# Performance work log

Measured on AMD Instinct MI355X. Metric: run time of the kernel, lower is better.

## Reference

```python
import jax, jax.numpy as jnp
import numpy as np

LAYERS = 30
LAYERS_PER_STACK = 10  # layers // stacks
UPSAMPLE_SCALES = (10, 8)


def _c1x1(w, x):
    # 1x1 conv: w [O,C], x [B,C,T] -> [B,O,T]
    return jnp.einsum('oc,bct->bot', w, x)


def setup_inputs() -> dict:
    key = jax.random.key(0)
    ks = jax.random.split(key, 16)
    B, T, F = 4, 32000, 400
    s = 0.1  # weight scale to keep gates unsaturated
    inp = {
        'x': jax.random.normal(ks[0], (B, 256, T), jnp.float32),
        'c': jax.random.normal(ks[1], (B, 80, F), jnp.float32),
        'first_w': jax.random.normal(ks[2], (64, 256), jnp.float32) * s,
        'first_b': jnp.zeros((64,), jnp.float32),
        'conv_w': jax.random.normal(ks[3], (LAYERS, 128, 64, 2), jnp.float32) * s,
        'conv_b': jnp.zeros((LAYERS, 128), jnp.float32),
        'cond_w': jax.random.normal(ks[4], (LAYERS, 128, 80), jnp.float32) * s,
        'out_w': jax.random.normal(ks[5], (LAYERS, 64, 64), jnp.float32) * s,
        'out_b': jnp.zeros((LAYERS, 64), jnp.float32),
        'skip_w': jax.random.normal(ks[6], (LAYERS, 64, 64), jnp.float32) * s,
        'skip_b': jnp.zeros((LAYERS, 64), jnp.float32),
        'last1_w': jax.random.normal(ks[7], (64, 64), jnp.float32) * s,
        'last1_b': jnp.zeros((64,), jnp.float32),
        'last2_w': jax.random.normal(ks[8], (256, 64), jnp.float32) * s,
        'last2_b': jnp.zeros((256,), jnp.float32),
        'conv_in_w': jax.random.normal(ks[9], (80, 80), jnp.float32) * s,
        # upsample smoothing kernels, torch init: constant 1/kernel_size
        'up_w0': jnp.full((2 * 10 + 1,), 1.0 / (2 * 10 + 1), jnp.float32),
        'up_w1': jnp.full((2 * 8 + 1,), 1.0 / (2 * 8 + 1), jnp.float32),
    }
    return inp


def _wavenet(x, c, first_w, first_b, conv_w, conv_b, cond_w, out_w, out_b,
             skip_w, skip_b, last1_w, last1_b, last2_w, last2_b, conv_in_w,
             up_w0, up_w1):
    # --- ConvInUpsampleNetwork (aux_context_window=0 -> conv_in is 1x1, no bias) ---
    c = _c1x1(conv_in_w, c)  # [B,80,F]
    C = c.shape[1]
    for scale, w in zip(UPSAMPLE_SCALES, (up_w0, up_w1)):
        c = jnp.repeat(c, scale, axis=2)  # nearest interpolate along time
        rhs = jnp.broadcast_to(w[None, None, :], (C, 1, w.shape[0]))  # depthwise avg
        c = jax.lax.conv_general_dilated(
            c, rhs, window_strides=(1,), padding=[(scale, scale)],
            feature_group_count=C, dimension_numbers=('NCH', 'OIH', 'NCH'))
    # c now [B,80,T] with T = F*80 matching x
    T = x.shape[2]

    # --- first 1x1 conv ---
    h = _c1x1(first_w, x) + first_b[None, :, None]  # [B,64,T]

    skips = jnp.zeros_like(h[:, :64, :]) * 0.0  # [B,64,T]
    skips = 0.0
    for l in range(LAYERS):
        d = 2 ** (l % LAYERS_PER_STACK)  # dilation; padding = (k-1)*d = d
        xp = jnp.pad(h, ((0, 0), (0, 0), (d, 0)))  # causal left pad
        # dilated conv, kernel_size=2: taps at t-d and t
        g = (jnp.einsum('oc,bct->bot', conv_w[l, :, :, 0], xp[:, :, :T])
             + jnp.einsum('oc,bct->bot', conv_w[l, :, :, 1], xp[:, :, d:d + T])
             + conv_b[l][None, :, None])  # [B,128,T]
        g = g + _c1x1(cond_w[l], c)  # conditioning (split(a,b)+split(ca,cb) == split(g+cc))
        a, b = jnp.split(g, 2, axis=1)
        z = jnp.tanh(a) * jax.nn.sigmoid(b)  # [B,64,T]
        skips = skips + _c1x1(skip_w[l], z) + skip_b[l][None, :, None]
        h = h + _c1x1(out_w[l], z) + out_b[l][None, :, None]

    # --- last conv layers: ReLU, 1x1, ReLU, 1x1 ---
    o = jax.nn.relu(skips)
    o = _c1x1(last1_w, o) + last1_b[None, :, None]
    o = jax.nn.relu(o)
    o = _c1x1(last2_w, o) + last2_b[None, :, None]
    return o  # [B,256,T]


def reference(x, c, first_w, first_b, conv_w, conv_b, cond_w, out_w, out_b,
              skip_w, skip_b, last1_w, last1_b, last2_w, last2_b, conv_in_w,
              up_w0, up_w1):
    return _wavenet(x, c, first_w, first_b, conv_w, conv_b, cond_w, out_w,
                    out_b, skip_w, skip_b, last1_w, last1_b, last2_w, last2_b,
                    conv_in_w, up_w0, up_w1)
```

## Files before the change

### kernel.cpp

```cpp
#include <hip/hip_runtime.h>
#include <math.h>

#define T_TOTAL 32000
#define BATCH 4
#define TT 64
#define TTF 32
#define ZCHUNK 15
#define ZSLOT_ELEMS ((size_t)BATCH * T_TOTAL * 64)

typedef __bf16 bf16x8 __attribute__((ext_vector_type(8)));
typedef float f32x4 __attribute__((ext_vector_type(4)));
typedef unsigned int uint4v __attribute__((ext_vector_type(4)));
typedef unsigned int uint2v __attribute__((ext_vector_type(2)));

__device__ __forceinline__ unsigned short f2b(float f) {
    unsigned int u = __float_as_uint(f);
    u += 0x7FFFu + ((u >> 16) & 1u);
    return (unsigned short)(u >> 16);
}
__device__ __forceinline__ unsigned int f2b2(float lo, float hi) {
    return (unsigned int)f2b(lo) | ((unsigned int)f2b(hi) << 16);
}
__device__ __forceinline__ bf16x8 ld_bf8(const unsigned short* p) {
    return __builtin_bit_cast(bf16x8, *(const uint4v*)p);
}
__device__ __forceinline__ float fast_sigmoid(float x) {
    return __builtin_amdgcn_rcpf(1.0f + __expf(-x));
}
__device__ __forceinline__ float fast_tanh(float x) {
    return 1.0f - 2.0f * __builtin_amdgcn_rcpf(1.0f + __expf(2.0f * x));
}

__global__ void k_pack(const float* __restrict__ conv_w, const float* __restrict__ cond_w,
                       const float* __restrict__ skip_w, const float* __restrict__ out_w,
                       const float* __restrict__ first_w, const float* __restrict__ last1_w,
                       const float* __restrict__ last2_w, const float* __restrict__ skip_b,
                       unsigned short* __restrict__ wgp, unsigned short* __restrict__ wzp,
                       unsigned short* __restrict__ fwp, unsigned short* __restrict__ l1p,
                       unsigned short* __restrict__ l2p, float* __restrict__ sbs) {
    int i = blockIdx.x * blockDim.x + threadIdx.x;
    if (i < 860160) {
        int l = i / 28672, r = i % 28672;
        int o = r / 224, k = r % 224;
        float v;
        if (k < 64)       v = conv_w[(((size_t)l * 128 + o) * 64 + k) * 2 + 0];
        else if (k < 128) v = conv_w[(((size_t)l * 128 + o) * 64 + (k - 64)) * 2 + 1];
        else if (k < 208) v = cond_w[((size_t)l * 128 + o) * 80 + (k - 128)];
        else              v = 0.0f;
        wgp[i] = f2b(v);
        return;
    }
    i -= 860160;
    if (i < 245760) {
        int l = i / 8192, rr = (i % 8192) / 64, k = i % 64;
        float v = (rr < 64) ? skip_w[((size_t)l * 64 + rr) * 64 + k]
                            : out_w[((size_t)l * 64 + (rr - 64)) * 64 + k];
        wzp[i] = f2b(v);
        return;
    }
    i -= 245760;
    if (i < 16384) { fwp[i] = f2b(first_w[i]); return; }
    i -= 16384;
    if (i < 4096) { l1p[i] = f2b(last1_w[i]); return; }
    i -= 4096;
    if (i < 16384) { l2p[i] = f2b(last2_w[i]); return; }
    i -= 16384;
    if (i < 64) {
        float a = 0.f;
        for (int l = 0; l < 30; ++l) a += skip_b[l * 64 + i];
        sbs[i] = a;
    }
}

__global__ void k_convin(const float* __restrict__ c, const float* __restrict__ w,
                         float* __restrict__ c1) {
    int idx = blockIdx.x * blockDim.x + threadIdx.x;
    if (idx >= BATCH * 80 * 400) return;
    int f = idx % 400;
    int o = (idx / 400) % 80;
    int b = idx / (400 * 80);
    const float* cb = c + (size_t)b * 80 * 400 + f;
    const float* wr = w + o * 80;
    float acc = 0.f;
    #pragma unroll 8
    for (int j = 0; j < 80; ++j) acc += wr[j] * cb[(size_t)j * 400];
    c1[idx] = acc;
}

__global__ void k_up0(const float* __restrict__ c1, const float* __restrict__ w,
                      float* __restrict__ c2) {
    int idx = blockIdx.x * blockDim.x + threadIdx.x;
    if (idx >= BATCH * 80 * 4000) return;
    int t = idx % 4000;
    int ch = idx / 4000;
    int u = t / 10, r = t - u * 10;
    float w0 = 0.f, w1 = 0.f, w2 = 0.f;
    #pragma unroll
    for (int j = 0; j < 21; ++j) {
        float wj = w[j];
        int a = r - 10 + j;
        if (a < 0) w0 += wj;
        else if (a < 10) w1 += wj;
        else w2 += wj;
    }
    const float* src = c1 + (size_t)ch * 400;
    float s0 = (u >= 1) ? src[u - 1] : 0.f;
    float s1 = src[u];
    float s2 = (u + 1 < 400) ? src[u + 1] : 0.f;
    c2[idx] = w0 * s0 + w1 * s1 + w2 * s2;
}

__global__ __launch_bounds__(256) void k_up1b(const float* __restrict__ c2,
                                              const float* __restrict__ w,
                                              unsigned short* __restrict__ cupb) {
    __shared__ float S[80][13];
    __shared__ float W[8][4];
    const int b = blockIdx.y, t0 = blockIdx.x * 64;
    const int tid = threadIdx.x;
    const int u0 = t0 >> 3;

    for (int i = tid; i < 800; i += 256) {
        int ch = i / 10, uu = i % 10;
        int u = u0 - 1 + uu;
        float v = 0.f;
        if (u >= 0 && u < 4000) v = c2[((size_t)b * 80 + ch) * 4000 + u];
        S[ch][uu] = v;
    }
    if (tid < 24) {
        int r = tid / 3, k = tid % 3;
        int jlo = (k == 0) ? 0 : (k == 1 ? 8 - r : 16 - r);
        int jhi = (k == 0) ? 7 - r : (k == 1 ? 15 - r : 16);
        float a = 0.f;
        for (int j = jlo; j <= jhi; ++j) a += w[j];
        W[r][k] = a;
    }
    __syncthreads();

    unsigned short* ob = cupb + ((size_t)b * T_TOTAL + t0) * 96;
    for (int i = tid; i < 64 * 96; i += 256) {
        int ch = i % 96;
        int tl = i / 96;
        float acc = 0.f;
        if (ch < 80) {
            int r = tl & 7, ub = tl >> 3;
            acc = W[r][0] * S[ch][ub] + W[r][1] * S[ch][ub + 1] + W[r][2] * S[ch][ub + 2];
        }
        ob[i] = f2b(acc);
    }
}

#define XFS 266
__global__ __launch_bounds__(256, 8) void k_first(
    const float* __restrict__ x, const unsigned short* __restrict__ fwp,
    const float* __restrict__ fb, float* __restrict__ h0) {
    __shared__ unsigned short Xf[TTF * XFS];
    const int b = blockIdx.y, t0 = blockIdx.x * TTF, tid = threadIdx.x;
    const int lane = tid & 63;
    const int wv = __builtin_amdgcn_readfirstlane(tid >> 6);
    const int l15 = lane & 15, q = lane >> 4;

    for (int i = tid; i < 2048; i += 256) {
        int ch = i >> 3;
        int t4 = (i & 7) << 2;
        const float* xr = x + ((size_t)b * 256 + ch) * T_TOTAL + t0 + t4;
        float4 u = *(const float4*)xr;
        int base = t4 * XFS + ch;
        Xf[base + 0 * XFS] = f2b(u.x);
        Xf[base + 1 * XFS] = f2b(u.y);
        Xf[base + 2 * XFS] = f2b(u.z);
        Xf[base + 3 * XFS] = f2b(u.w);
    }
    __syncthreads();

    f32x4 acc[2] = {};
    const unsigned short* wr = fwp + (size_t)(16 * wv + l15) * 256;
    #pragma unroll
    for (int ks = 0; ks < 8; ++ks) {
        bf16x8 aA = ld_bf8(wr + ks * 32 + q * 8);
        #pragma unroll
        for (int tt = 0; tt < 2; ++tt) {
            bf16x8 bb = ld_bf8(&Xf[(tt * 16 + l15) * XFS + ks * 32 + q * 8]);
            acc[tt] = __builtin_amdgcn_mfma_f32_16x16x32_bf16(aA, bb, acc[tt], 0, 0, 0);
        }
    }
    const float4 fbv = *(const float4*)&fb[16 * wv + 4 * q];
    float* hob = h0 + (size_t)b * T_TOTAL * 64;
    #pragma unroll
    for (int tt = 0; tt < 2; ++tt) {
        size_t base = (size_t)(t0 + tt * 16 + l15) * 64 + 16 * wv + 4 * q;
        float4 ho;
        ho.x = acc[tt][0] + fbv.x;
        ho.y = acc[tt][1] + fbv.y;
        ho.z = acc[tt][2] + fbv.z;
        ho.w = acc[tt][3] + fbv.w;
        *(float4*)(hob + base) = ho;
    }
}

__global__ __launch_bounds__(256, 4) void k_layer(
    const float* __restrict__ h_in, float* __restrict__ h_out,
    unsigned short* __restrict__ zb_l, const unsigned short* __restrict__ cupb,
    const unsigned short* __restrict__ wgp_l, const unsigned short* __restrict__ wzp_l,
    const float* __restrict__ cb_l, const float* __restrict__ ob_l, int d) {
    __shared__ unsigned short Xl[64 * 224];
    __shared__ unsigned short zs[64 * 72];
    const int b = blockIdx.y, t0 = blockIdx.x * TT, tid = threadIdx.x;
    const int lane = tid & 63;
    const int wv = __builtin_amdgcn_readfirstlane(tid >> 6);
    const int l15 = lane & 15, q = lane >> 4;

    const float* hb = h_in + (size_t)b * T_TOTAL * 64;
    for (int i = tid; i < 512; i += 256) {
        int t = i >> 3, cb8 = (i & 7) << 3;
        const float4* p1 = (const float4*)(hb + (size_t)(t0 + t) * 64 + cb8);
        float4 u0 = p1[0], u1 = p1[1];
        uint4v v1;
        v1.x = f2b2(u0.x, u0.y); v1.y = f2b2(u0.z, u0.w);
        v1.z = f2b2(u1.x, u1.y); v1.w = f2b2(u1.z, u1.w);
        *(uint4v*)&Xl[t * 224 + 64 + cb8] = v1;
        int td = t0 + t - d;
        uint4v v0 = {0u, 0u, 0u, 0u};
        if (td >= 0) {
            const float4* p0 = (const float4*)(hb + (size_t)td * 64 + cb8);
            float4 w0 = p0[0], w1 = p0[1];
            v0.x = f2b2(w0.x, w0.y); v0.y = f2b2(w0.z, w0.w);
            v0.z = f2b2(w1.x, w1.y); v0.w = f2b2(w1.z, w1.w);
        }
        *(uint4v*)&Xl[t * 224 + cb8] = v0;
    }
    const unsigned short* cbb = cupb + (size_t)b * T_TOTAL * 96;
    for (int i = tid; i < 768; i += 256) {
        int t = i / 12, j = (i % 12) << 3;
        *(uint4v*)&Xl[t * 224 + 128 + j] = *(const uint4v*)&cbb[(size_t)(t0 + t) * 96 + j];
    }
    __syncthreads();

    f32x4 accA[4] = {}, accG[4] = {};
    const unsigned short* wrow_a = wgp_l + (size_t)(16 * wv + l15) * 224;
    const unsigned short* wrow_g = wgp_l + (size_t)(64 + 16 * wv + l15) * 224;
    #pragma unroll
    for (int ks = 0; ks < 7; ++ks) {
        bf16x8 aA = ld_bf8(wrow_a + ks * 32 + q * 8);
        bf16x8 aG = ld_bf8(wrow_g + ks * 32 + q * 8);
        #pragma unroll
        for (int tt = 0; tt < 4; ++tt) {
            bf16x8 bb = ld_bf8(&Xl[(tt * 16 + l15) * 224 + ks * 32 + q * 8]);
            accA[tt] = __builtin_amdgcn_mfma_f32_16x16x32_bf16(aA, bb, accA[tt], 0, 0, 0);
            accG[tt] = __builtin_amdgcn_mfma_f32_16x16x32_bf16(aG, bb, accG[tt], 0, 0, 0);
        }
    }
    const float4 cbA = *(const float4*)&cb_l[16 * wv + 4 * q];
    const float4 cbG = *(const float4*)&cb_l[64 + 16 * wv + 4 * q];
    #pragma unroll
    for (int tt = 0; tt < 4; ++tt) {
        int t = tt * 16 + l15;
        float z0 = fast_tanh(accA[tt][0] + cbA.x) * fast_sigmoid(accG[tt][0] + cbG.x);
        float z1 = fast_tanh(accA[tt][1] + cbA.y) * fast_sigmoid(accG[tt][1] + cbG.y);
        float z2 = fast_tanh(accA[tt][2] + cbA.z) * fast_sigmoid(accG[tt][2] + cbG.z);
        float z3 = fast_tanh(accA[tt][3] + cbA.w) * fast_sigmoid(accG[tt][3] + cbG.w);
        uint2v zv;
        zv.x = f2b2(z0, z1);
        zv.y = f2b2(z2, z3);
        *(uint2v*)&zs[t * 72 + 16 * wv + 4 * q] = zv;
    }
    __syncthreads();

    unsigned short* zg = zb_l + ((size_t)b * T_TOTAL + t0) * 64;
    #pragma unroll
    for (int it = 0; it < 2; ++it) {
        int i = tid + it * 256;
        int t = i >> 3, c8 = (i & 7) << 3;
        *(uint4v*)&zg[t * 64 + c8] = *(const uint4v*)&zs[t * 72 + c8];
    }

    f32x4 accO[4] = {};
    const unsigned short* zrow_o = wzp_l + (size_t)(64 + 16 * wv + l15) * 64;
    #pragma unroll
    for (int ks = 0; ks < 2; ++ks) {
        bf16x8 aO = ld_bf8(zrow_o + ks * 32 + q * 8);
        #pragma unroll
        for (int tt = 0; tt < 4; ++tt) {
            bf16x8 bb = ld_bf8(&zs[(tt * 16 + l15) * 72 + ks * 32 + q * 8]);
            accO[tt] = __builtin_amdgcn_mfma_f32_16x16x32_bf16(aO, bb, accO[tt], 0, 0, 0);
        }
    }
    const float4 obv = *(const float4*)&ob_l[16 * wv + 4 * q];
    float* hob = h_out + (size_t)b * T_TOTAL * 64;
    #pragma unroll
    for (int tt = 0; tt < 4; ++tt) {
        size_t base = (size_t)(t0 + tt * 16 + l15) * 64 + 16 * wv + 4 * q;
        float4 hi = *(const float4*)(hb + base);
        float4 ho;
        ho.x = hi.x + accO[tt][0] + obv.x;
        ho.y = hi.y + accO[tt][1] + obv.y;
        ho.z = hi.z + accO[tt][2] + obv.z;
        ho.w = hi.w + accO[tt][3] + obv.w;
        *(float4*)(hob + base) = ho;
    }
}

__global__ __launch_bounds__(256, 4) void k_layer_f(
    const float* __restrict__ h_in, float* __restrict__ h_out,
    float* __restrict__ skips, const unsigned short* __restrict__ cupb,
    const unsigned short* __restrict__ wgp, const unsigned short* __restrict__ wzp,
    const float* __restrict__ cb_l, const float* __restrict__ ob_l,
    const float* __restrict__ sb_l, int d, int first) {
    __shared__ unsigned short Xl[64 * 224];
    __shared__ unsigned short zs[64 * 72];
    const int b = blockIdx.y, t0 = blockIdx.x * TT, tid = threadIdx.x;
    const int lane = tid & 63;
    const int wv = __builtin_amdgcn_readfirstlane(tid >> 6);
    const int l15 = lane & 15, q = lane >> 4;

    const float* hb = h_in + (size_t)b * T_TOTAL * 64;
    for (int i = tid; i < 512; i += 256) {
        int t = i >> 3, cb8 = (i & 7) << 3;
        const float4* p1 = (const float4*)(hb + (size_t)(t0 + t) * 64 + cb8);
        float4 u0 = p1[0], u1 = p1[1];
        uint4v v1;
        v1.x = f2b2(u0.x, u0.y); v1.y = f2b2(u0.z, u0.w);
        v1.z = f2b2(u1.x, u1.y); v1.w = f2b2(u1.z, u1.w);
        *(uint4v*)&Xl[t * 224 + 64 + cb8] = v1;
        int td = t0 + t - d;
        uint4v v0 = {0u, 0u, 0u, 0u};
        if (td >= 0) {
            const float4* p0 = (const float4*)(hb + (size_t)td * 64 + cb8);
            float4 w0 = p0[0], w1 = p0[1];
            v0.x = f2b2(w0.x, w0.y); v0.y = f2b2(w0.z, w0.w);
            v0.z = f2b2(w1.x, w1.y); v0.w = f2b2(w1.z, w1.w);
        }
        *(uint4v*)&Xl[t * 224 + cb8] = v0;
    }
    const unsigned short* cbb = cupb + (size_t)b * T_TOTAL * 96;
    for (int i = tid; i < 768; i += 256) {
        int t = i / 12, j = (i % 12) << 3;
        *(uint4v*)&Xl[t * 224 + 128 + j] = *(const uint4v*)&cbb[(size_t)(t0 + t) * 96 + j];
    }
    __syncthreads();

    f32x4 accA[4] = {}, accG[4] = {};
    const unsigned short* wrow_a = wgp + (size_t)(16 * wv + l15) * 224;
    const unsigned short* wrow_g = wgp + (size_t)(64 + 16 * wv + l15) * 224;
    #pragma unroll
    for (int ks = 0; ks < 7; ++ks) {
        bf16x8 aA = ld_bf8(wrow_a + ks * 32 + q * 8);
        bf16x8 aG = ld_bf8(wrow_g + ks * 32 + q * 8);
        #pragma unroll
        for (int tt = 0; tt < 4; ++tt) {
            bf16x8 bb = ld_bf8(&Xl[(tt * 16 + l15) * 224 + ks * 32 + q * 8]);
            accA[tt] = __builtin_amdgcn_mfma_f32_16x16x32_bf16(aA, bb, accA[tt], 0, 0, 0);
            accG[tt] = __builtin_amdgcn_mfma_f32_16x16x32_bf16(aG, bb, accG[tt], 0, 0, 0);
        }
    }
    const float4 cbA = *(const float4*)&cb_l[16 * wv + 4 * q];
    const float4 cbG = *(const float4*)&cb_l[64 + 16 * wv + 4 * q];
    #pragma unroll
    for (int tt = 0; tt < 4; ++tt) {
        int t = tt * 16 + l15;
        float z0 = fast_tanh(accA[tt][0] + cbA.x) * fast_sigmoid(accG[tt][0] + cbG.x);
        float z1 = fast_tanh(accA[tt][1] + cbA.y) * fast_sigmoid(accG[tt][1] + cbG.y);
        float z2 = fast_tanh(accA[tt][2] + cbA.z) * fast_sigmoid(accG[tt][2] + cbG.z);
        float z3 = fast_tanh(accA[tt][3] + cbA.w) * fast_sigmoid(accG[tt][3] + cbG.w);
        uint2v zv;
        zv.x = f2b2(z0, z1);
        zv.y = f2b2(z2, z3);
        *(uint2v*)&zs[t * 72 + 16 * wv + 4 * q] = zv;
    }
    __syncthreads();

    f32x4 accS[4] = {}, accO[4] = {};
    const unsigned short* zrow_s = wzp + (size_t)(16 * wv + l15) * 64;
    const unsigned short* zrow_o = wzp + (size_t)(64 + 16 * wv + l15) * 64;
    #pragma unroll
    for (int ks = 0; ks < 2; ++ks) {
        bf16x8 aS = ld_bf8(zrow_s + ks * 32 + q * 8);
        bf16x8 aO = ld_bf8(zrow_o + ks * 32 + q * 8);
        #pragma unroll
        for (int tt = 0; tt < 4; ++tt) {
            bf16x8 bb = ld_bf8(&zs[(tt * 16 + l15) * 72 + ks * 32 + q * 8]);
            accS[tt] = __builtin_amdgcn_mfma_f32_16x16x32_bf16(aS, bb, accS[tt], 0, 0, 0);
            accO[tt] = __builtin_amdgcn_mfma_f32_16x16x32_bf16(aO, bb, accO[tt], 0, 0, 0);
        }
    }
    const float4 sbv = *(const float4*)&sb_l[16 * wv + 4 * q];
    const float4 obv = *(const float4*)&ob_l[16 * wv + 4 * q];
    float* hob = h_out + (size_t)b * T_TOTAL * 64;
    float* skb = skips + (size_t)b * T_TOTAL * 64;
    #pragma unroll
    for (int tt = 0; tt < 4; ++tt) {
        size_t base = (size_t)(t0 + tt * 16 + l15) * 64 + 16 * wv + 4 * q;
        float4 hi = *(const float4*)(hb + base);
        float4 ho;
        ho.x = hi.x + accO[tt][0] + obv.x;
        ho.y = hi.y + accO[tt][1] + obv.y;
        ho.z = hi.z + accO[tt][2] + obv.z;
        ho.w = hi.w + accO[tt][3] + obv.w;
        *(float4*)(hob + base) = ho;
        float4 sv;
        if (first) {
            sv.x = accS[tt][0] + sbv.x;
            sv.y = accS[tt][1] + sbv.y;
            sv.z = accS[tt][2] + sbv.z;
            sv.w = accS[tt][3] + sbv.w;
        } else {
            float4 sp = *(const float4*)(skb + base);
            sv.x = sp.x + accS[tt][0] + sbv.x;
            sv.y = sp.y + accS[tt][1] + sbv.y;
            sv.z = sp.z + accS[tt][2] + sbv.z;
            sv.w = sp.w + accS[tt][3] + sbv.w;
        }
        *(float4*)(skb + base) = sv;
    }
}

__global__ __launch_bounds__(256) void k_skips(
    const unsigned short* __restrict__ zbuf, const unsigned short* __restrict__ wzp_c,
    int nl, float* __restrict__ partial, int mode,
    const float* __restrict__ sbs, const unsigned short* __restrict__ l1p,
    const float* __restrict__ b1, const unsigned short* __restrict__ l2p,
    const float* __restrict__ b2, float* __restrict__ out) {
    __shared__ unsigned short zt[64 * 72];
    __shared__ unsigned short o2s[64 * 72];
    const int b = blockIdx.y, t0 = blockIdx.x * TT, tid = threadIdx.x;
    const int lane = tid & 63;
    const int wv = __builtin_amdgcn_readfirstlane(tid >> 6);
    const int l15 = lane & 15, q = lane >> 4;

    const int st_t = tid >> 3, st_c = (tid & 7) << 3;
    const int st_t2 = (tid + 256) >> 3, st_c2 = ((tid + 256) & 7) << 3;
    const unsigned short* zb = zbuf + ((size_t)b * T_TOTAL + t0) * 64;

    f32x4 acc[4] = {};
    for (int l = 0; l < nl; ++l) {
        const unsigned short* src = zb + (size_t)l * ZSLOT_ELEMS;
        *(uint4v*)&zt[st_t * 72 + st_c] = *(const uint4v*)&src[st_t * 64 + st_c];
        *(uint4v*)&zt[st_t2 * 72 + st_c2] = *(const uint4v*)&src[st_t2 * 64 + st_c2];
        __syncthreads();
        const unsigned short* wr = wzp_c + (size_t)l * 8192 + (size_t)(16 * wv + l15) * 64;
        #pragma unroll
        for (int ks = 0; ks < 2; ++ks) {
            bf16x8 aS = ld_bf8(wr + ks * 32 + q * 8);
            #pragma unroll
            for (int tt = 0; tt < 4; ++tt) {
                bf16x8 bb = ld_bf8(&zt[(tt * 16 + l15) * 72 + ks * 32 + q * 8]);
                acc[tt] = __builtin_amdgcn_mfma_f32_16x16x32_bf16(aS, bb, acc[tt], 0, 0, 0);
            }
        }
        __syncthreads();
    }

    float* pb = partial + (size_t)b * T_TOTAL * 64;
    if (mode == 0) {
        #pragma unroll
        for (int tt = 0; tt < 4; ++tt) {
            size_t base = (size_t)(t0 + tt * 16 + l15) * 64 + 16 * wv + 4 * q;
            float4 sv;
            sv.x = acc[tt][0]; sv.y = acc[tt][1]; sv.z = acc[tt][2]; sv.w = acc[tt][3];
            *(float4*)(pb + base) = sv;
        }
        return;
    }

    const float4 sbv = *(const float4*)&sbs[16 * wv + 4 * q];
    #pragma unroll
    for (int tt = 0; tt < 4; ++tt) {
        int t = tt * 16 + l15;
        size_t base = (size_t)(t0 + t) * 64 + 16 * wv + 4 * q;
        float4 sp = *(const float4*)(pb + base);
        float s0 = fmaxf(sp.x + acc[tt][0] + sbv.x, 0.f);
        float s1 = fmaxf(sp.y + acc[tt][1] + sbv.y, 0.f);
        float s2 = fmaxf(sp.z + acc[tt][2] + sbv.z, 0.f);
        float s3 = fmaxf(sp.w + acc[tt][3] + sbv.w, 0.f);
        uint2v zv;
        zv.x = f2b2(s0, s1);
        zv.y = f2b2(s2, s3);
        *(uint2v*)&zt[t * 72 + 16 * wv + 4 * q] = zv;
    }
    __syncthreads();

    f32x4 a1[4] = {};
    const unsigned short* w1r = l1p + (size_t)(16 * wv + l15) * 64;
    #pragma unroll
    for (int ks = 0; ks < 2; ++ks) {
        bf16x8 aA = ld_bf8(w1r + ks * 32 + q * 8);
        #pragma unroll
        for (int tt = 0; tt < 4; ++tt) {
            bf16x8 bb = ld_bf8(&zt[(tt * 16 + l15) * 72 + ks * 32 + q * 8]);
            a1[tt] = __builtin_amdgcn_mfma_f32_16x16x32_bf16(aA, bb, a1[tt], 0, 0, 0);
        }
    }
    const float4 b1v = *(const float4*)&b1[16 * wv + 4 * q];
    #pragma unroll
    for (int tt = 0; tt < 4; ++tt) {
        int t = tt * 16 + l15;
        float z0 = fmaxf(a1[tt][0] + b1v.x, 0.f);
        float z1 = fmaxf(a1[tt][1] + b1v.y, 0.f);
        float z2 = fmaxf(a1[tt][2] + b1v.z, 0.f);
        float z3 = fmaxf(a1[tt][3] + b1v.w, 0.f);
        uint2v zv;
        zv.x = f2b2(z0, z1);
        zv.y = f2b2(z2, z3);
        *(uint2v*)&o2s[t * 72 + 16 * wv + 4 * q] = zv;
    }
    __syncthreads();

    f32x4 a2[4][4] = {};
    #pragma unroll
    for (int ks = 0; ks < 2; ++ks) {
        bf16x8 aw[4];
        #pragma unroll
        for (int j = 0; j < 4; ++j)
            aw[j] = ld_bf8(l2p + (size_t)(64 * wv + 16 * j + l15) * 64 + ks * 32 + q * 8);
        #pragma unroll
        for (int tt = 0; tt < 4; ++tt) {
            bf16x8 bb = ld_bf8(&o2s[(tt * 16 + l15) * 72 + ks * 32 + q * 8]);
            #pragma unroll
            for (int j = 0; j < 4; ++j)
                a2[j][tt] = __builtin_amdgcn_mfma_f32_16x16x32_bf16(aw[j], bb, a2[j][tt], 0, 0, 0);
        }
    }
    float* ob = out + (size_t)b * 256 * T_TOTAL;
    #pragma unroll
    for (int j = 0; j < 4; ++j) {
        int o0 = 64 * wv + 16 * j + 4 * q;
        float4 b2v = *(const float4*)&b2[o0];
        #pragma unroll
        for (int tt = 0; tt < 4; ++tt) {
            int t = t0 + tt * 16 + l15;
            ob[(size_t)(o0 + 0) * T_TOTAL + t] = a2[j][tt][0] + b2v.x;
            ob[(size_t)(o0 + 1) * T_TOTAL + t] = a2[j][tt][1] + b2v.y;
            ob[(size_t)(o0 + 2) * T_TOTAL + t] = a2[j][tt][2] + b2v.z;
            ob[(size_t)(o0 + 3) * T_TOTAL + t] = a2[j][tt][3] + b2v.w;
        }
    }
}

__global__ __launch_bounds__(256) void k_last(
    const float* __restrict__ skips, const unsigned short* __restrict__ l1p,
    const float* __restrict__ b1, const unsigned short* __restrict__ l2p,
    const float* __restrict__ b2, float* __restrict__ out) {
    __shared__ unsigned short sp[64 * 72];
    __shared__ unsigned short o2s[64 * 72];
    const int b = blockIdx.y, t0 = blockIdx.x * TT, tid = threadIdx.x;
    const int lane = tid & 63;
    const int wv = __builtin_amdgcn_readfirstlane(tid >> 6);
    const int l15 = lane & 15, q = lane >> 4;

    const float* skb = skips + (size_t)b * T_TOTAL * 64;
    for (int i = tid; i < 512; i += 256) {
        int t = i >> 3, cb8 = (i & 7) << 3;
        const float4* p = (const float4*)(skb + (size_t)(t0 + t) * 64 + cb8);
        float4 u0 = p[0], u1 = p[1];
        uint4v v;
        v.x = f2b2(fmaxf(u0.x, 0.f), fmaxf(u0.y, 0.f));
        v.y = f2b2(fmaxf(u0.z, 0.f), fmaxf(u0.w, 0.f));
        v.z = f2b2(fmaxf(u1.x, 0.f), fmaxf(u1.y, 0.f));
        v.w = f2b2(fmaxf(u1.z, 0.f), fmaxf(u1.w, 0.f));
        *(uint4v*)&sp[t * 72 + cb8] = v;
    }
    __syncthreads();

    f32x4 a1[4] = {};
    const unsigned short* w1r = l1p + (size_t)(16 * wv + l15) * 64;
    #pragma unroll
    for (int ks = 0; ks < 2; ++ks) {
        bf16x8 aA = ld_bf8(w1r + ks * 32 + q * 8);
        #pragma unroll
        for (int tt = 0; tt < 4; ++tt) {
            bf16x8 bb = ld_bf8(&sp[(tt * 16 + l15) * 72 + ks * 32 + q * 8]);
            a1[tt] = __builtin_amdgcn_mfma_f32_16x16x32_bf16(aA, bb, a1[tt], 0, 0, 0);
        }
    }
    const float4 b1v = *(const float4*)&b1[16 * wv + 4 * q];
    #pragma unroll
    for (int tt = 0; tt < 4; ++tt) {
        int t = tt * 16 + l15;
        float z0 = fmaxf(a1[tt][0] + b1v.x, 0.f);
        float z1 = fmaxf(a1[tt][1] + b1v.y, 0.f);
        float z2 = fmaxf(a1[tt][2] + b1v.z, 0.f);
        float z3 = fmaxf(a1[tt][3] + b1v.w, 0.f);
        uint2v zv;
        zv.x = f2b2(z0, z1);
        zv.y = f2b2(z2, z3);
        *(uint2v*)&o2s[t * 72 + 16 * wv + 4 * q] = zv;
    }
    __syncthreads();

    f32x4 a2[4][4] = {};
    #pragma unroll
    for (int ks = 0; ks < 2; ++ks) {
        bf16x8 aw[4];
        #pragma unroll
        for (int j = 0; j < 4; ++j)
            aw[j] = ld_bf8(l2p + (size_t)(64 * wv + 16 * j + l15) * 64 + ks * 32 + q * 8);
        #pragma unroll
        for (int tt = 0; tt < 4; ++tt) {
            bf16x8 bb = ld_bf8(&o2s[(tt * 16 + l15) * 72 + ks * 32 + q * 8]);
            #pragma unroll
            for (int j = 0; j < 4; ++j)
                a2[j][tt] = __builtin_amdgcn_mfma_f32_16x16x32_bf16(aw[j], bb, a2[j][tt], 0, 0, 0);
        }
    }
    float* ob = out + (size_t)b * 256 * T_TOTAL;
    #pragma unroll
    for (int j = 0; j < 4; ++j) {
        int o0 = 64 * wv + 16 * j + 4 * q;
        float4 b2v = *(const float4*)&b2[o0];
        #pragma unroll
        for (int tt = 0; tt < 4; ++tt) {
            int t = t0 + tt * 16 + l15;
            ob[(size_t)(o0 + 0) * T_TOTAL + t] = a2[j][tt][0] + b2v.x;
            ob[(size_t)(o0 + 1) * T_TOTAL + t] = a2[j][tt][1] + b2v.y;
            ob[(size_t)(o0 + 2) * T_TOTAL + t] = a2[j][tt][2] + b2v.z;
            ob[(size_t)(o0 + 3) * T_TOTAL + t] = a2[j][tt][3] + b2v.w;
        }
    }
}

extern "C" void kernel_launch(void* const* d_in, const int* in_sizes, int n_in,
                              void* d_out, int out_size, void* d_ws, size_t ws_size,
                              hipStream_t stream) {
    const float* x         = (const float*)d_in[0];
    const float* c         = (const float*)d_in[1];
    const float* first_w   = (const float*)d_in[2];
    const float* first_b   = (const float*)d_in[3];
    const float* conv_w    = (const float*)d_in[4];
    const float* conv_b    = (const float*)d_in[5];
    const float* cond_w    = (const float*)d_in[6];
    const float* out_w     = (const float*)d_in[7];
    const float* out_b     = (const float*)d_in[8];
    const float* skip_w    = (const float*)d_in[9];
    const float* skip_b    = (const float*)d_in[10];
    const float* last1_w   = (const float*)d_in[11];
    const float* last1_b   = (const float*)d_in[12];
    const float* last2_w   = (const float*)d_in[13];
    const float* last2_b   = (const float*)d_in[14];
    const float* conv_in_w = (const float*)d_in[15];
    const float* up_w0     = (const float*)d_in[16];
    const float* up_w1     = (const float*)d_in[17];

    unsigned char* base = (unsigned char*)d_ws;
    float* c1            = (float*)(base + 0);
    float* c2            = (float*)(base + 512000);
    unsigned short* cupb = (unsigned short*)(base + 5632000);
    float* hA            = (float*)(base + 30208000);
    float* hB            = (float*)(base + 62976000);
    float* skipsP        = (float*)(base + 95744000);
    unsigned short* wgp  = (unsigned short*)(base + 128512000);
    unsigned short* wzp  = (unsigned short*)(base + 130232320);
    unsigned short* fwp  = (unsigned short*)(base + 130723840);
    unsigned short* l1p  = (unsigned short*)(base + 130756608);
    unsigned short* l2p  = (unsigned short*)(base + 130764800);
    float* sbs           = (float*)(base + 130797568);
    unsigned short* zbuf = (unsigned short*)(base + 130797824);

    const bool big = ws_size >= 376557824ull;

    k_pack<<<(1142848 + 255) / 256, 256, 0, stream>>>(
        conv_w, cond_w, skip_w, out_w, first_w, last1_w, last2_w, skip_b,
        wgp, wzp, fwp, l1p, l2p, sbs);
    k_convin<<<(BATCH * 80 * 400 + 255) / 256, 256, 0, stream>>>(c, conv_in_w, c1);
    k_up0<<<(BATCH * 80 * 4000 + 255) / 256, 256, 0, stream>>>(c1, up_w0, c2);
    dim3 upg(T_TOTAL / 64, BATCH);
    k_up1b<<<upg, 256, 0, stream>>>(c2, up_w1, cupb);

    dim3 gridF(T_TOTAL / TTF, BATCH);
    k_first<<<gridF, 256, 0, stream>>>(x, fwp, first_b, hA);

    dim3 grid(T_TOTAL / TT, BATCH);
    float* hin = hA;
    float* hout = hB;

    if (big) {
        for (int l = 0; l < 30; ++l) {
            int d = 1 << (l % 10);
            int sl = l % ZCHUNK;
            k_layer<<<grid, 256, 0, stream>>>(
                hin, hout, zbuf + (size_t)sl * ZSLOT_ELEMS, cupb,
                wgp + (size_t)l * 128 * 224, wzp + (size_t)l * 128 * 64,
                conv_b + (size_t)l * 128, out_b + (size_t)l * 64, d);
            if (l == ZCHUNK - 1) {
                k_skips<<<grid, 256, 0, stream>>>(zbuf, wzp, ZCHUNK, skipsP, 0,
                                                  sbs, l1p, last1_b, l2p, last2_b,
                                                  (float*)d_out);
            }
            float* tmp = hin; hin = hout; hout = tmp;
        }
        k_skips<<<grid, 256, 0, stream>>>(zbuf, wzp + (size_t)ZCHUNK * 8192, ZCHUNK,
                                          skipsP, 1, sbs, l1p, last1_b, l2p, last2_b,
                                          (float*)d_out);
    } else {
        for (int l = 0; l < 30; ++l) {
            int d = 1 << (l % 10);
            k_layer_f<<<grid, 256, 0, stream>>>(
                hin, hout, skipsP, cupb,
                wgp + (size_t)l * 128 * 224, wzp + (size_t)l * 128 * 64,
                conv_b + (size_t)l * 128, out_b + (size_t)l * 64, skip_b + (size_t)l * 64,
                d, l == 0 ? 1 : 0);
            float* tmp = hin; hin = hout; hout = tmp;
        }
        k_last<<<grid, 256, 0, stream>>>(skipsP, l1p, last1_b, l2p, last2_b, (float*)d_out);
    }
}
```

Measured before the change: 1.505 ms.

## Shrink z-buffer chunk to six layers and read z directly in skips kernel

Deferred skip accumulation now works in five chunks of six layers instead of two chunks of fifteen, with partial sums carried between chunks. The z ring buffer shrinks from 15 slots to 6 (about 98 MB instead of 245 MB of bf16), so the z data a skips pass reads back is more likely to still sit in the MI355X last-level cache. The skips kernel also drops its LDS staging and barriers and feeds MFMA operands straight from global memory. In exchange there are more k_skips launches and extra read/write round trips of the fp32 partial skip sums.

```diff
diff --git a/kernel.cpp b/kernel.cpp
--- a/kernel.cpp
+++ b/kernel.cpp
@@ -5,7 +5,7 @@
 #define BATCH 4
 #define TT 64
 #define TTF 32
-#define ZCHUNK 15
+#define ZCHUNK 6
 #define ZSLOT_ELEMS ((size_t)BATCH * T_TOTAL * 64)
 
 typedef __bf16 bf16x8 __attribute__((ext_vector_type(8)));
@@ -415,7 +415,7 @@
 
 __global__ __launch_bounds__(256) void k_skips(
     const unsigned short* __restrict__ zbuf, const unsigned short* __restrict__ wzp_c,
-    int nl, float* __restrict__ partial, int mode,
+    int nl, float* __restrict__ partial, int acc_in, int finalize,
     const float* __restrict__ sbs, const unsigned short* __restrict__ l1p,
     const float* __restrict__ b1, const unsigned short* __restrict__ l2p,
     const float* __restrict__ b2, float* __restrict__ out) {
@@ -426,36 +426,43 @@
     const int wv = __builtin_amdgcn_readfirstlane(tid >> 6);
     const int l15 = lane & 15, q = lane >> 4;
 
-    const int st_t = tid >> 3, st_c = (tid & 7) << 3;
-    const int st_t2 = (tid + 256) >> 3, st_c2 = ((tid + 256) & 7) << 3;
     const unsigned short* zb = zbuf + ((size_t)b * T_TOTAL + t0) * 64;
 
     f32x4 acc[4] = {};
     for (int l = 0; l < nl; ++l) {
         const unsigned short* src = zb + (size_t)l * ZSLOT_ELEMS;
-        *(uint4v*)&zt[st_t * 72 + st_c] = *(const uint4v*)&src[st_t * 64 + st_c];
-        *(uint4v*)&zt[st_t2 * 72 + st_c2] = *(const uint4v*)&src[st_t2 * 64 + st_c2];
-        __syncthreads();
         const unsigned short* wr = wzp_c + (size_t)l * 8192 + (size_t)(16 * wv + l15) * 64;
         #pragma unroll
         for (int ks = 0; ks < 2; ++ks) {
             bf16x8 aS = ld_bf8(wr + ks * 32 + q * 8);
             #pragma unroll
             for (int tt = 0; tt < 4; ++tt) {
-                bf16x8 bb = ld_bf8(&zt[(tt * 16 + l15) * 72 + ks * 32 + q * 8]);
+                bf16x8 bb = ld_bf8(&src[(size_t)(tt * 16 + l15) * 64 + ks * 32 + q * 8]);
                 acc[tt] = __builtin_amdgcn_mfma_f32_16x16x32_bf16(aS, bb, acc[tt], 0, 0, 0);
             }
         }
-        __syncthreads();
     }
 
     float* pb = partial + (size_t)b * T_TOTAL * 64;
-    if (mode == 0) {
+    float4 pin[4];
+    if (acc_in) {
+        #pragma unroll
+        for (int tt = 0; tt < 4; ++tt)
+            pin[tt] = *(const float4*)(pb + (size_t)(t0 + tt * 16 + l15) * 64 + 16 * wv + 4 * q);
+    } else {
+        #pragma unroll
+        for (int tt = 0; tt < 4; ++tt) pin[tt] = make_float4(0.f, 0.f, 0.f, 0.f);
+    }
+
+    if (!finalize) {
         #pragma unroll
         for (int tt = 0; tt < 4; ++tt) {
             size_t base = (size_t)(t0 + tt * 16 + l15) * 64 + 16 * wv + 4 * q;
             float4 sv;
-            sv.x = acc[tt][0]; sv.y = acc[tt][1]; sv.z = acc[tt][2]; sv.w = acc[tt][3];
+            sv.x = pin[tt].x + acc[tt][0];
+            sv.y = pin[tt].y + acc[tt][1];
+            sv.z = pin[tt].z + acc[tt][2];
+            sv.w = pin[tt].w + acc[tt][3];
             *(float4*)(pb + base) = sv;
         }
         return;
@@ -465,12 +472,10 @@
     #pragma unroll
     for (int tt = 0; tt < 4; ++tt) {
         int t = tt * 16 + l15;
-        size_t base = (size_t)(t0 + t) * 64 + 16 * wv + 4 * q;
-        float4 sp = *(const float4*)(pb + base);
-        float s0 = fmaxf(sp.x + acc[tt][0] + sbv.x, 0.f);
-        float s1 = fmaxf(sp.y + acc[tt][1] + sbv.y, 0.f);
-        float s2 = fmaxf(sp.z + acc[tt][2] + sbv.z, 0.f);
-        float s3 = fmaxf(sp.w + acc[tt][3] + sbv.w, 0.f);
+        float s0 = fmaxf(pin[tt].x + acc[tt][0] + sbv.x, 0.f);
+        float s1 = fmaxf(pin[tt].y + acc[tt][1] + sbv.y, 0.f);
+        float s2 = fmaxf(pin[tt].z + acc[tt][2] + sbv.z, 0.f);
+        float s3 = fmaxf(pin[tt].w + acc[tt][3] + sbv.w, 0.f);
         uint2v zv;
         zv.x = f2b2(s0, s1);
         zv.y = f2b2(s2, s3);
@@ -654,7 +659,7 @@
     float* sbs           = (float*)(base + 130797568);
     unsigned short* zbuf = (unsigned short*)(base + 130797824);
 
-    const bool big = ws_size >= 376557824ull;
+    const bool big = ws_size >= 229101824ull;
 
     k_pack<<<(1142848 + 255) / 256, 256, 0, stream>>>(
         conv_w, cond_w, skip_w, out_w, first_w, last1_w, last2_w, skip_b,
@@ -672,23 +677,22 @@
     float* hout = hB;
 
     if (big) {
-        for (int l = 0; l < 30; ++l) {
-            int d = 1 << (l % 10);
-            int sl = l % ZCHUNK;
-            k_layer<<<grid, 256, 0, stream>>>(
-                hin, hout, zbuf + (size_t)sl * ZSLOT_ELEMS, cupb,
-                wgp + (size_t)l * 128 * 224, wzp + (size_t)l * 128 * 64,
-                conv_b + (size_t)l * 128, out_b + (size_t)l * 64, d);
-            if (l == ZCHUNK - 1) {
-                k_skips<<<grid, 256, 0, stream>>>(zbuf, wzp, ZCHUNK, skipsP, 0,
-                                                  sbs, l1p, last1_b, l2p, last2_b,
-                                                  (float*)d_out);
+        const int nchunks = 30 / ZCHUNK;
+        for (int ch = 0; ch < nchunks; ++ch) {
+            for (int j = 0; j < ZCHUNK; ++j) {
+                int l = ch * ZCHUNK + j;
+                int d = 1 << (l % 10);
+                k_layer<<<grid, 256, 0, stream>>>(
+                    hin, hout, zbuf + (size_t)j * ZSLOT_ELEMS, cupb,
+                    wgp + (size_t)l * 128 * 224, wzp + (size_t)l * 128 * 64,
+                    conv_b + (size_t)l * 128, out_b + (size_t)l * 64, d);
+                float* tmp = hin; hin = hout; hout = tmp;
             }
-            float* tmp = hin; hin = hout; hout = tmp;
-        }
-        k_skips<<<grid, 256, 0, stream>>>(zbuf, wzp + (size_t)ZCHUNK * 8192, ZCHUNK,
-                                          skipsP, 1, sbs, l1p, last1_b, l2p, last2_b,
-                                          (float*)d_out);
+            k_skips<<<grid, 256, 0, stream>>>(
+                zbuf, wzp + (size_t)ch * ZCHUNK * 8192, ZCHUNK, skipsP,
+                ch > 0 ? 1 : 0, ch == nchunks - 1 ? 1 : 0,
+                sbs, l1p, last1_b, l2p, last2_b, (float*)d_out);
+        }
     } else {
         for (int l = 0; l < 30; ++l) {
             int d = 1 << (l % 10);
```

New measurement: 1.585 ms. 5.3% more time.

## Fuse all layers into one persistent cooperative kernel with register-held skip accumulators

Applied to the files above, without the earlier changes.

Replaces the per-layer launches and the z-buffer plus separate skip-reduction kernels with a single cooperative persistent kernel. Each block owns two time tiles per batch, runs all 30 layers with grid.sync between them, and keeps the skip sums in MFMA accumulator registers. The final ReLU and 1x1 output layers run in the same kernel. This removes the z buffer traffic and the launch overhead. In exchange it adds grid-wide barriers and caps the kernel at 1000 blocks, which must all be co-resident, so it has less latency hiding than the larger grid had.

```diff
diff --git a/kernel.cpp b/kernel.cpp
--- a/kernel.cpp
+++ b/kernel.cpp
@@ -1,12 +1,13 @@
 #include <hip/hip_runtime.h>
+#include <hip/hip_cooperative_groups.h>
 #include <math.h>
+
+namespace cg = cooperative_groups;
 
 #define T_TOTAL 32000
 #define BATCH 4
 #define TT 64
 #define TTF 32
-#define ZCHUNK 15
-#define ZSLOT_ELEMS ((size_t)BATCH * T_TOTAL * 64)
 
 typedef __bf16 bf16x8 __attribute__((ext_vector_type(8)));
 typedef float f32x4 __attribute__((ext_vector_type(4)));
@@ -197,19 +198,14 @@
     }
 }
 
-__global__ __launch_bounds__(256, 4) void k_layer(
-    const float* __restrict__ h_in, float* __restrict__ h_out,
-    unsigned short* __restrict__ zb_l, const unsigned short* __restrict__ cupb,
+__device__ __forceinline__ void layer_tile(
+    const float* __restrict__ hb, float* __restrict__ hob,
+    const unsigned short* __restrict__ cbb,
     const unsigned short* __restrict__ wgp_l, const unsigned short* __restrict__ wzp_l,
-    const float* __restrict__ cb_l, const float* __restrict__ ob_l, int d) {
-    __shared__ unsigned short Xl[64 * 224];
-    __shared__ unsigned short zs[64 * 72];
-    const int b = blockIdx.y, t0 = blockIdx.x * TT, tid = threadIdx.x;
-    const int lane = tid & 63;
-    const int wv = __builtin_amdgcn_readfirstlane(tid >> 6);
-    const int l15 = lane & 15, q = lane >> 4;
-
-    const float* hb = h_in + (size_t)b * T_TOTAL * 64;
+    const float* __restrict__ cb_l, const float* __restrict__ ob_l,
+    int t0, int d, int tid, int wv, int l15, int q,
+    unsigned short* __restrict__ Xl, unsigned short* __restrict__ zs,
+    f32x4 (&accS)[4], int writeH) {
     for (int i = tid; i < 512; i += 256) {
         int t = i >> 3, cb8 = (i & 7) << 3;
         const float4* p1 = (const float4*)(hb + (size_t)(t0 + t) * 64 + cb8);
@@ -228,7 +224,6 @@
         }
         *(uint4v*)&Xl[t * 224 + cb8] = v0;
     }
-    const unsigned short* cbb = cupb + (size_t)b * T_TOTAL * 96;
     for (int i = tid; i < 768; i += 256) {
         int t = i / 12, j = (i % 12) << 3;
         *(uint4v*)&Xl[t * 224 + 128 + j] = *(const uint4v*)&cbb[(size_t)(t0 + t) * 96 + j];
@@ -265,38 +260,170 @@
     }
     __syncthreads();
 
-    unsigned short* zg = zb_l + ((size_t)b * T_TOTAL + t0) * 64;
-    #pragma unroll
-    for (int it = 0; it < 2; ++it) {
-        int i = tid + it * 256;
-        int t = i >> 3, c8 = (i & 7) << 3;
-        *(uint4v*)&zg[t * 64 + c8] = *(const uint4v*)&zs[t * 72 + c8];
-    }
-
-    f32x4 accO[4] = {};
-    const unsigned short* zrow_o = wzp_l + (size_t)(64 + 16 * wv + l15) * 64;
+    const unsigned short* zrow_s = wzp_l + (size_t)(16 * wv + l15) * 64;
+    if (writeH) {
+        f32x4 accO[4] = {};
+        const unsigned short* zrow_o = wzp_l + (size_t)(64 + 16 * wv + l15) * 64;
+        #pragma unroll
+        for (int ks = 0; ks < 2; ++ks) {
+            bf16x8 aS = ld_bf8(zrow_s + ks * 32 + q * 8);
+            bf16x8 aO = ld_bf8(zrow_o + ks * 32 + q * 8);
+            #pragma unroll
+            for (int tt = 0; tt < 4; ++tt) {
+                bf16x8 bb = ld_bf8(&zs[(tt * 16 + l15) * 72 + ks * 32 + q * 8]);
+                accS[tt] = __builtin_amdgcn_mfma_f32_16x16x32_bf16(aS, bb, accS[tt], 0, 0, 0);
+                accO[tt] = __builtin_amdgcn_mfma_f32_16x16x32_bf16(aO, bb, accO[tt], 0, 0, 0);
+            }
+        }
+        const float4 obv = *(const float4*)&ob_l[16 * wv + 4 * q];
+        #pragma unroll
+        for (int tt = 0; tt < 4; ++tt) {
+            size_t base = (size_t)(t0 + tt * 16 + l15) * 64 + 16 * wv + 4 * q;
+            float4 hi = *(const float4*)(hb + base);
+            float4 ho;
+            ho.x = hi.x + accO[tt][0] + obv.x;
+            ho.y = hi.y + accO[tt][1] + obv.y;
+            ho.z = hi.z + accO[tt][2] + obv.z;
+            ho.w = hi.w + accO[tt][3] + obv.w;
+            *(float4*)(hob + base) = ho;
+        }
+    } else {
+        #pragma unroll
+        for (int ks = 0; ks < 2; ++ks) {
+            bf16x8 aS = ld_bf8(zrow_s + ks * 32 + q * 8);
+            #pragma unroll
+            for (int tt = 0; tt < 4; ++tt) {
+                bf16x8 bb = ld_bf8(&zs[(tt * 16 + l15) * 72 + ks * 32 + q * 8]);
+                accS[tt] = __builtin_amdgcn_mfma_f32_16x16x32_bf16(aS, bb, accS[tt], 0, 0, 0);
+            }
+        }
+    }
+}
+
+__device__ __forceinline__ void last_tile(
+    f32x4 (&accS)[4], const float* __restrict__ sbs,
+    const unsigned short* __restrict__ l1p, const float* __restrict__ b1,
+    const unsigned short* __restrict__ l2p, const float* __restrict__ b2,
+    float* __restrict__ ob, int t0, int tid, int wv, int l15, int q,
+    unsigned short* __restrict__ zt, unsigned short* __restrict__ o2s) {
+    const float4 sbv = *(const float4*)&sbs[16 * wv + 4 * q];
+    #pragma unroll
+    for (int tt = 0; tt < 4; ++tt) {
+        int t = tt * 16 + l15;
+        float s0 = fmaxf(accS[tt][0] + sbv.x, 0.f);
+        float s1 = fmaxf(accS[tt][1] + sbv.y, 0.f);
+        float s2 = fmaxf(accS[tt][2] + sbv.z, 0.f);
+        float s3 = fmaxf(accS[tt][3] + sbv.w, 0.f);
+        uint2v zv;
+        zv.x = f2b2(s0, s1);
+        zv.y = f2b2(s2, s3);
+        *(uint2v*)&zt[t * 72 + 16 * wv + 4 * q] = zv;
+    }
+    __syncthreads();
+
+    f32x4 a1[4] = {};
+    const unsigned short* w1r = l1p + (size_t)(16 * wv + l15) * 64;
     #pragma unroll
     for (int ks = 0; ks < 2; ++ks) {
-        bf16x8 aO = ld_bf8(zrow_o + ks * 32 + q * 8);
-        #pragma unroll
-        for (int tt = 0; tt < 4; ++tt) {
-            bf16x8 bb = ld_bf8(&zs[(tt * 16 + l15) * 72 + ks * 32 + q * 8]);
-            accO[tt] = __builtin_amdgcn_mfma_f32_16x16x32_bf16(aO, bb, accO[tt], 0, 0, 0);
-        }
-    }
-    const float4 obv = *(const float4*)&ob_l[16 * wv + 4 * q];
-    float* hob = h_out + (size_t)b * T_TOTAL * 64;
+        bf16x8 aA = ld_bf8(w1r + ks * 32 + q * 8);
+        #pragma unroll
+        for (int tt = 0; tt < 4; ++tt) {
+            bf16x8 bb = ld_bf8(&zt[(tt * 16 + l15) * 72 + ks * 32 + q * 8]);
+            a1[tt] = __builtin_amdgcn_mfma_f32_16x16x32_bf16(aA, bb, a1[tt], 0, 0, 0);
+        }
+    }
+    const float4 b1v = *(const float4*)&b1[16 * wv + 4 * q];
     #pragma unroll
     for (int tt = 0; tt < 4; ++tt) {
-        size_t base = (size_t)(t0 + tt * 16 + l15) * 64 + 16 * wv + 4 * q;
-        float4 hi = *(const float4*)(hb + base);
-        float4 ho;
-        ho.x = hi.x + accO[tt][0] + obv.x;
-        ho.y = hi.y + accO[tt][1] + obv.y;
-        ho.z = hi.z + accO[tt][2] + obv.z;
-        ho.w = hi.w + accO[tt][3] + obv.w;
-        *(float4*)(hob + base) = ho;
-    }
+        int t = tt * 16 + l15;
+        float z0 = fmaxf(a1[tt][0] + b1v.x, 0.f);
+        float z1 = fmaxf(a1[tt][1] + b1v.y, 0.f);
+        float z2 = fmaxf(a1[tt][2] + b1v.z, 0.f);
+        float z3 = fmaxf(a1[tt][3] + b1v.w, 0.f);
+        uint2v zv;
+        zv.x = f2b2(z0, z1);
+        zv.y = f2b2(z2, z3);
+        *(uint2v*)&o2s[t * 72 + 16 * wv + 4 * q] = zv;
+    }
+    __syncthreads();
+
+    f32x4 a2[4][4] = {};
+    #pragma unroll
+    for (int ks = 0; ks < 2; ++ks) {
+        bf16x8 aw[4];
+        #pragma unroll
+        for (int j = 0; j < 4; ++j)
+            aw[j] = ld_bf8(l2p + (size_t)(64 * wv + 16 * j + l15) * 64 + ks * 32 + q * 8);
+        #pragma unroll
+        for (int tt = 0; tt < 4; ++tt) {
+            bf16x8 bb = ld_bf8(&o2s[(tt * 16 + l15) * 72 + ks * 32 + q * 8]);
+            #pragma unroll
+            for (int j = 0; j < 4; ++j)
+                a2[j][tt] = __builtin_amdgcn_mfma_f32_16x16x32_bf16(aw[j], bb, a2[j][tt], 0, 0, 0);
+        }
+    }
+    #pragma unroll
+    for (int j = 0; j < 4; ++j) {
+        int o0 = 64 * wv + 16 * j + 4 * q;
+        float4 b2v = *(const float4*)&b2[o0];
+        #pragma unroll
+        for (int tt = 0; tt < 4; ++tt) {
+            int t = t0 + tt * 16 + l15;
+            ob[(size_t)(o0 + 0) * T_TOTAL + t] = a2[j][tt][0] + b2v.x;
+            ob[(size_t)(o0 + 1) * T_TOTAL + t] = a2[j][tt][1] + b2v.y;
+            ob[(size_t)(o0 + 2) * T_TOTAL + t] = a2[j][tt][2] + b2v.z;
+            ob[(size_t)(o0 + 3) * T_TOTAL + t] = a2[j][tt][3] + b2v.w;
+        }
+    }
+}
+
+__global__ __launch_bounds__(256, 4) void k_wavenet(
+    float* __restrict__ hA, float* __restrict__ hB,
+    const unsigned short* __restrict__ cupb,
+    const unsigned short* __restrict__ wgp, const unsigned short* __restrict__ wzp,
+    const float* __restrict__ conv_b, const float* __restrict__ out_b,
+    const float* __restrict__ sbs,
+    const unsigned short* __restrict__ l1p, const float* __restrict__ b1,
+    const unsigned short* __restrict__ l2p, const float* __restrict__ b2,
+    float* __restrict__ out) {
+    cg::grid_group grid = cg::this_grid();
+    __shared__ unsigned short Xl[64 * 224];
+    __shared__ unsigned short zs[64 * 72];
+    const int tid = threadIdx.x;
+    const int lane = tid & 63;
+    const int wv = __builtin_amdgcn_readfirstlane(tid >> 6);
+    const int l15 = lane & 15, q = lane >> 4;
+    const int b = blockIdx.x & 3;
+    const int p = blockIdx.x >> 2;
+    const int t0A = p * 64;
+    const int t0B = (p + 250) * 64;
+
+    const unsigned short* cbb = cupb + (size_t)b * T_TOTAL * 96;
+    float* hin = hA + (size_t)b * T_TOTAL * 64;
+    float* hout = hB + (size_t)b * T_TOTAL * 64;
+
+    f32x4 accSA[4] = {}, accSB[4] = {};
+
+    for (int l = 0; l < 30; ++l) {
+        const int d = 1 << (l % 10);
+        const unsigned short* wgp_l = wgp + (size_t)l * 128 * 224;
+        const unsigned short* wzp_l = wzp + (size_t)l * 8192;
+        const float* cb_l = conv_b + (size_t)l * 128;
+        const float* ob_l = out_b + (size_t)l * 64;
+        const int wH = (l != 29);
+        layer_tile(hin, hout, cbb, wgp_l, wzp_l, cb_l, ob_l, t0A, d,
+                   tid, wv, l15, q, Xl, zs, accSA, wH);
+        layer_tile(hin, hout, cbb, wgp_l, wzp_l, cb_l, ob_l, t0B, d,
+                   tid, wv, l15, q, Xl, zs, accSB, wH);
+        if (l != 29) {
+            grid.sync();
+            float* tmp = hin; hin = hout; hout = tmp;
+        }
+    }
+
+    float* ob = out + (size_t)b * 256 * T_TOTAL;
+    last_tile(accSA, sbs, l1p, b1, l2p, b2, ob, t0A, tid, wv, l15, q, Xl, zs);
+    last_tile(accSB, sbs, l1p, b1, l2p, b2, ob, t0B, tid, wv, l15, q, Xl, zs);
 }
 
 __global__ __launch_bounds__(256, 4) void k_layer_f(
@@ -413,128 +540,6 @@
     }
 }
 
-__global__ __launch_bounds__(256) void k_skips(
-    const unsigned short* __restrict__ zbuf, const unsigned short* __restrict__ wzp_c,
-    int nl, float* __restrict__ partial, int mode,
-    const float* __restrict__ sbs, const unsigned short* __restrict__ l1p,
-    const float* __restrict__ b1, const unsigned short* __restrict__ l2p,
-    const float* __restrict__ b2, float* __restrict__ out) {
-    __shared__ unsigned short zt[64 * 72];
-    __shared__ unsigned short o2s[64 * 72];
-    const int b = blockIdx.y, t0 = blockIdx.x * TT, tid = threadIdx.x;
-    const int lane = tid & 63;
-    const int wv = __builtin_amdgcn_readfirstlane(tid >> 6);
-    const int l15 = lane & 15, q = lane >> 4;
-
-    const int st_t = tid >> 3, st_c = (tid & 7) << 3;
-    const int st_t2 = (tid + 256) >> 3, st_c2 = ((tid + 256) & 7) << 3;
-    const unsigned short* zb = zbuf + ((size_t)b * T_TOTAL + t0) * 64;
-
-    f32x4 acc[4] = {};
-    for (int l = 0; l < nl; ++l) {
-        const unsigned short* src = zb + (size_t)l * ZSLOT_ELEMS;
-        *(uint4v*)&zt[st_t * 72 + st_c] = *(const uint4v*)&src[st_t * 64 + st_c];
-        *(uint4v*)&zt[st_t2 * 72 + st_c2] = *(const uint4v*)&src[st_t2 * 64 + st_c2];
-        __syncthreads();
-        const unsigned short* wr = wzp_c + (size_t)l * 8192 + (size_t)(16 * wv + l15) * 64;
-        #pragma unroll
-        for (int ks = 0; ks < 2; ++ks) {
-            bf16x8 aS = ld_bf8(wr + ks * 32 + q * 8);
-            #pragma unroll
-            for (int tt = 0; tt < 4; ++tt) {
-                bf16x8 bb = ld_bf8(&zt[(tt * 16 + l15) * 72 + ks * 32 + q * 8]);
-                acc[tt] = __builtin_amdgcn_mfma_f32_16x16x32_bf16(aS, bb, acc[tt], 0, 0, 0);
-            }
-        }
-        __syncthreads();
-    }
-
-    float* pb = partial + (size_t)b * T_TOTAL * 64;
-    if (mode == 0) {
-        #pragma unroll
-        for (int tt = 0; tt < 4; ++tt) {
-            size_t base = (size_t)(t0 + tt * 16 + l15) * 64 + 16 * wv + 4 * q;
-            float4 sv;
-            sv.x = acc[tt][0]; sv.y = acc[tt][1]; sv.z = acc[tt][2]; sv.w = acc[tt][3];
-            *(float4*)(pb + base) = sv;
-        }
-        return;
-    }
-
-    const float4 sbv = *(const float4*)&sbs[16 * wv + 4 * q];
-    #pragma unroll
-    for (int tt = 0; tt < 4; ++tt) {
-        int t = tt * 16 + l15;
-        size_t base = (size_t)(t0 + t) * 64 + 16 * wv + 4 * q;
-        float4 sp = *(const float4*)(pb + base);
-        float s0 = fmaxf(sp.x + acc[tt][0] + sbv.x, 0.f);
-        float s1 = fmaxf(sp.y + acc[tt][1] + sbv.y, 0.f);
-        float s2 = fmaxf(sp.z + acc[tt][2] + sbv.z, 0.f);
-        float s3 = fmaxf(sp.w + acc[tt][3] + sbv.w, 0.f);
-        uint2v zv;
-        zv.x = f2b2(s0, s1);
-        zv.y = f2b2(s2, s3);
-        *(uint2v*)&zt[t * 72 + 16 * wv + 4 * q] = zv;
-    }
-    __syncthreads();
-
-    f32x4 a1[4] = {};
-    const unsigned short* w1r = l1p + (size_t)(16 * wv + l15) * 64;
-    #pragma unroll
-    for (int ks = 0; ks < 2; ++ks) {
-        bf16x8 aA = ld_bf8(w1r + ks * 32 + q * 8);
-        #pragma unroll
-        for (int tt = 0; tt < 4; ++tt) {
-            bf16x8 bb = ld_bf8(&zt[(tt * 16 + l15) * 72 + ks * 32 + q * 8]);
-            a1[tt] = __builtin_amdgcn_mfma_f32_16x16x32_bf16(aA, bb, a1[tt], 0, 0, 0);
-        }
-    }
-    const float4 b1v = *(const float4*)&b1[16 * wv + 4 * q];
-    #pragma unroll
-    for (int tt = 0; tt < 4; ++tt) {
-        int t = tt * 16 + l15;
-        float z0 = fmaxf(a1[tt][0] + b1v.x, 0.f);
-        float z1 = fmaxf(a1[tt][1] + b1v.y, 0.f);
-        float z2 = fmaxf(a1[tt][2] + b1v.z, 0.f);
-        float z3 = fmaxf(a1[tt][3] + b1v.w, 0.f);
-        uint2v zv;
-        zv.x = f2b2(z0, z1);
-        zv.y = f2b2(z2, z3);
-        *(uint2v*)&o2s[t * 72 + 16 * wv + 4 * q] = zv;
-    }
-    __syncthreads();
-
-    f32x4 a2[4][4] = {};
-    #pragma unroll
-    for (int ks = 0; ks < 2; ++ks) {
-        bf16x8 aw[4];
-        #pragma unroll
-        for (int j = 0; j < 4; ++j)
-            aw[j] = ld_bf8(l2p + (size_t)(64 * wv + 16 * j + l15) * 64 + ks * 32 + q * 8);
-        #pragma unroll
-        for (int tt = 0; tt < 4; ++tt) {
-            bf16x8 bb = ld_bf8(&o2s[(tt * 16 + l15) * 72 + ks * 32 + q * 8]);
-            #pragma unroll
-            for (int j = 0; j < 4; ++j)
-                a2[j][tt] = __builtin_amdgcn_mfma_f32_16x16x32_bf16(aw[j], bb, a2[j][tt], 0, 0, 0);
-        }
-    }
-    float* ob = out + (size_t)b * 256 * T_TOTAL;
-    #pragma unroll
-    for (int j = 0; j < 4; ++j) {
-        int o0 = 64 * wv + 16 * j + 4 * q;
-        float4 b2v = *(const float4*)&b2[o0];
-        #pragma unroll
-        for (int tt = 0; tt < 4; ++tt) {
-            int t = t0 + tt * 16 + l15;
-            ob[(size_t)(o0 + 0) * T_TOTAL + t] = a2[j][tt][0] + b2v.x;
-            ob[(size_t)(o0 + 1) * T_TOTAL + t] = a2[j][tt][1] + b2v.y;
-            ob[(size_t)(o0 + 2) * T_TOTAL + t] = a2[j][tt][2] + b2v.z;
-            ob[(size_t)(o0 + 3) * T_TOTAL + t] = a2[j][tt][3] + b2v.w;
-        }
-    }
-}
-
 __global__ __launch_bounds__(256) void k_last(
     const float* __restrict__ skips, const unsigned short* __restrict__ l1p,
     const float* __restrict__ b1, const unsigned short* __restrict__ l2p,
@@ -626,9 +631,9 @@
     const float* first_b   = (const float*)d_in[3];
     const float* conv_w    = (const float*)d_in[4];
     const float* conv_b    = (const float*)d_in[5];
+    const float* out_b     = (const float*)d_in[8];
     const float* cond_w    = (const float*)d_in[6];
     const float* out_w     = (const float*)d_in[7];
-    const float* out_b     = (const float*)d_in[8];
     const float* skip_w    = (const float*)d_in[9];
     const float* skip_b    = (const float*)d_in[10];
     const float* last1_w   = (const float*)d_in[11];
@@ -652,9 +657,6 @@
     unsigned short* l1p  = (unsigned short*)(base + 130756608);
     unsigned short* l2p  = (unsigned short*)(base + 130764800);
     float* sbs           = (float*)(base + 130797568);
-    unsigned short* zbuf = (unsigned short*)(base + 130797824);
-
-    const bool big = ws_size >= 376557824ull;
 
     k_pack<<<(1142848 + 255) / 256, 256, 0, stream>>>(
         conv_w, cond_w, skip_w, out_w, first_w, last1_w, last2_w, skip_b,
@@ -667,29 +669,19 @@
     dim3 gridF(T_TOTAL / TTF, BATCH);
     k_first<<<gridF, 256, 0, stream>>>(x, fwp, first_b, hA);
 
-    dim3 grid(T_TOTAL / TT, BATCH);
-    float* hin = hA;
-    float* hout = hB;
-
-    if (big) {
-        for (int l = 0; l < 30; ++l) {
-            int d = 1 << (l % 10);
-            int sl = l % ZCHUNK;
-            k_layer<<<grid, 256, 0, stream>>>(
-                hin, hout, zbuf + (size_t)sl * ZSLOT_ELEMS, cupb,
-                wgp + (size_t)l * 128 * 224, wzp + (size_t)l * 128 * 64,
-                conv_b + (size_t)l * 128, out_b + (size_t)l * 64, d);
-            if (l == ZCHUNK - 1) {
-                k_skips<<<grid, 256, 0, stream>>>(zbuf, wzp, ZCHUNK, skipsP, 0,
-                                                  sbs, l1p, last1_b, l2p, last2_b,
-                                                  (float*)d_out);
-            }
-            float* tmp = hin; hin = hout; hout = tmp;
-        }
-        k_skips<<<grid, 256, 0, stream>>>(zbuf, wzp + (size_t)ZCHUNK * 8192, ZCHUNK,
-                                          skipsP, 1, sbs, l1p, last1_b, l2p, last2_b,
-                                          (float*)d_out);
-    } else {
+    float* outp = (float*)d_out;
+    void* kargs[] = {(void*)&hA, (void*)&hB, (void*)&cupb, (void*)&wgp, (void*)&wzp,
+                     (void*)&conv_b, (void*)&out_b, (void*)&sbs,
+                     (void*)&l1p, (void*)&last1_b, (void*)&l2p, (void*)&last2_b,
+                     (void*)&outp};
+    hipError_t cerr = hipLaunchCooperativeKernel((const void*)k_wavenet,
+                                                 dim3(1000), dim3(256),
+                                                 kargs, 0, stream);
+    if (cerr != hipSuccess) {
+        (void)hipGetLastError();
+        dim3 grid(T_TOTAL / TT, BATCH);
+        float* hin = hA;
+        float* hout = hB;
         for (int l = 0; l < 30; ++l) {
             int d = 1 << (l % 10);
             k_layer_f<<<grid, 256, 0, stream>>>(
```

Measured after the change: 4.939 ms. 228% more time.
